# Optimization experiments

Measured on AMD Instinct MI355X. Metric: run time of the kernel, lower is better.

## Reference

```python
import jax, jax.numpy as jnp
import numpy as np
import jax.scipy.linalg

BATCH = 1048576
M_NUM = 2
DT = 0.0166667
NN_RATIO = 0.5
SLOPE = 0.01  # torch LeakyReLU default negative_slope


def setup_inputs() -> dict:
    key = jax.random.key(0)
    ks = jax.random.split(key, 16)
    inp = {}
    inp["SS"] = jax.random.normal(ks[0], (BATCH, 2), dtype=jnp.float32)
    inp["Alphas"] = jax.random.uniform(ks[1], (BATCH, M_NUM), dtype=jnp.float32)
    # per-muscle scalar parameters (positive so sqrt(K*I) is valid)
    inp["K0s"] = jax.random.uniform(ks[2], (M_NUM,), minval=0.5, maxval=1.5)
    inp["K1s"] = jax.random.uniform(ks[3], (M_NUM,), minval=0.5, maxval=1.5)
    inp["L0s"] = jax.random.uniform(ks[4], (M_NUM,), minval=0.5, maxval=1.5)
    inp["L1s"] = jax.random.uniform(ks[5], (M_NUM,), minval=0.1, maxval=0.6)
    inp["Ms"] = jnp.array([1.0, -1.0], dtype=jnp.float32)  # moment arms
    inp["I_p"] = jnp.array([1.0], dtype=jnp.float32)
    inp["B_p"] = jnp.array([0.05], dtype=jnp.float32)
    inp["K_p"] = jnp.array([1.0], dtype=jnp.float32)
    # per-muscle compensational MLP weights: 3-32-32-32-1 (eval mode, dropout off)
    s = 0.1
    inp["W1"] = jax.random.normal(ks[6], (M_NUM, 3, 32)) * s
    inp["b1"] = jax.random.normal(ks[7], (M_NUM, 32)) * s
    inp["W2"] = jax.random.normal(ks[8], (M_NUM, 32, 32)) * s
    inp["b2"] = jax.random.normal(ks[9], (M_NUM, 32)) * s
    inp["W3"] = jax.random.normal(ks[10], (M_NUM, 32, 32)) * s
    inp["b3"] = jax.random.normal(ks[11], (M_NUM, 32)) * s
    inp["W4"] = jax.random.normal(ks[12], (M_NUM, 32, 1)) * s
    inp["b4"] = jax.random.normal(ks[13], (M_NUM, 1)) * s
    return inp


def _leaky(x):
    return jnp.where(x >= 0, x, SLOPE * x)


def reference(SS, Alphas, K0s, K1s, L0s, L1s, Ms, I_p, B_p, K_p,
              W1, b1, W2, b2, W3, b3, W4, b4):
    B = SS.shape[0]
    a = jnp.clip(Alphas, 0.0, 1.0)                      # (B, m)
    # muscle length / speed via scalar moment arms
    l = SS[:, 0:1] * Ms[None, :]                        # (B, m)
    dl = SS[:, 1:2] * Ms[None, :]                       # (B, m)
    # compensational MLPs, vectorized over muscles
    x = jnp.stack([l, dl, a], axis=-1)                  # (B, m, 3)
    h = _leaky(jnp.einsum('bmi,mio->bmo', x, W1) + b1[None])
    h = _leaky(jnp.einsum('bmi,mio->bmo', h, W2) + b2[None])
    h = _leaky(jnp.einsum('bmi,mio->bmo', h, W3) + b3[None])
    nn_out = jnp.tanh(jnp.einsum('bmi,mio->bmo', h, W4) + b4[None])[..., 0] * NN_RATIO  # (B, m)

    I0, B0p, K0p = I_p[0], B_p[0], K_p[0]
    K_m = K0s[None, :] + K1s[None, :] * a               # (B, m)
    K_tot = jnp.sum(K_m * Ms[None, :] ** 2, axis=1)     # (B,)
    A10 = -(K_tot + K0p) / I0
    D = 2.0 * jnp.sqrt(K_tot * I0)
    A11 = -(D + B0p) / I0
    B_F = K_m * (L0s[None, :] + L1s[None, :] * a - jnp.abs(l)) \
        + K1s[None, :] * L1s[None, :] * a * a * nn_out   # (B, m)
    B10 = jnp.sum(B_F * Ms[None, :], axis=1) / I0       # (B,)

    # Build block matrix M6 = [[A*dt, B*dt, 0], [0, 0, I2], [0, 0, 0]]
    M6 = jnp.zeros((B, 6, 6), dtype=SS.dtype)
    M6 = M6.at[:, 0, 1].set(DT)
    M6 = M6.at[:, 1, 0].set(A10 * DT)
    M6 = M6.at[:, 1, 1].set(A11 * DT)
    M6 = M6.at[:, 1, 2].set(B10 * DT)
    M6 = M6.at[:, 1, 3].set(DT / I0)
    M6 = M6.at[:, 2, 4].set(1.0)
    M6 = M6.at[:, 3, 5].set(1.0)

    expMT = jax.vmap(jax.scipy.linalg.expm)(M6)         # (B, 6, 6)
    Ad = expMT[:, :2, :2]
    Bd1 = expMT[:, :2, 4:6]
    Bd0 = expMT[:, :2, 2:4] - Bd1
    u = jnp.array([1.0, 0.0], dtype=SS.dtype)           # U0 = U1 = [1, 0]
    SSout = (jnp.einsum('bij,bj->bi', Ad, SS)
             + jnp.einsum('bij,j->bi', Bd0, u)
             + jnp.einsum('bij,j->bi', Bd1, u))          # (B, 2)
    return SSout[:, :1], SSout
```

## Files before the change

kernel.cpp:

```cpp
#include <hip/hip_runtime.h>
#include <hip/hip_bf16.h>

#define NTHREADS 256
#define WAVES    4
#define GPW      4
#define DT_F     0.0166667f

typedef _Float16 f16x8 __attribute__((ext_vector_type(8)));
typedef _Float16 f16x4 __attribute__((ext_vector_type(4)));
typedef _Float16 f16x2 __attribute__((ext_vector_type(2)));
typedef float    f32x4 __attribute__((ext_vector_type(4)));

#define BF16_PROBE 0xBF803F80u

#define OW1 0
#define OB1 192
#define OW2 256
#define OB2 2368
#define OW3 2432
#define OB3 4544
#define OW4 4608
#define OB4 4672
#define SMEM_F 4680

__device__ __forceinline__ float leaky(float x) { return fmaxf(x, 0.01f * x); }

__device__ __forceinline__ float tanh_fast(float x) {
    const float xc = fminf(fmaxf(x, -10.0f), 10.0f);
    const float t  = __expf(2.0f * xc);
    return (t - 1.0f) * __builtin_amdgcn_rcpf(t + 1.0f);
}

__device__ __forceinline__ f16x2 pkrtz(float a, float b) {
    return __builtin_bit_cast(f16x2, __builtin_amdgcn_cvt_pkrtz(a, b));
}

__device__ __forceinline__ f16x4 leaky_cvt(const f32x4 D) {
    f16x2 lo = pkrtz(D[0], D[1]);
    f16x2 hi = pkrtz(D[2], D[3]);
    const f16x2 sl = {(_Float16)0.01f, (_Float16)0.01f};
    lo = __builtin_elementwise_max(lo, lo * sl);
    hi = __builtin_elementwise_max(hi, hi * sl);
    return __builtin_shufflevector(lo, hi, 0, 1, 2, 3);
}

__device__ __forceinline__ f16x4 bias_leaky_cvt(const f32x4 D, const f16x4 b) {
    f16x2 lo = pkrtz(D[0], D[1]);
    f16x2 hi = pkrtz(D[2], D[3]);
    const f16x2 blo = {b[0], b[1]};
    const f16x2 bhi = {b[2], b[3]};
    lo = lo + blo;
    hi = hi + bhi;
    const f16x2 sl = {(_Float16)0.01f, (_Float16)0.01f};
    lo = __builtin_elementwise_max(lo, lo * sl);
    hi = __builtin_elementwise_max(hi, hi * sl);
    return __builtin_shufflevector(lo, hi, 0, 1, 2, 3);
}

__device__ __forceinline__ f16x8 concat8(const f16x4 a, const f16x4 b) {
    return __builtin_shufflevector(a, b, 0, 1, 2, 3, 4, 5, 6, 7);
}

__device__ __forceinline__ void epilogue_math(
    const float* P, float ss0, float ss1, float a0, float a1,
    float nn0, float nn1, float& o0f, float& o1f)
{
    const float K00 = P[0], K01 = P[1], K10 = P[2], K11 = P[3];
    const float L00 = P[4], L01 = P[5], L10 = P[6], L11 = P[7];
    const float Ms0 = P[8], Ms1 = P[9];
    const float I0  = P[10], B0p = P[11], K0p = P[12];

    const float Km0   = fmaf(K10, a0, K00);
    const float Km1   = fmaf(K11, a1, K01);
    const float K_tot = Km0*Ms0*Ms0 + Km1*Ms1*Ms1;
    const float invI  = 1.0f / I0;
    const float A10   = -(K_tot + K0p) * invI;
    const float Dd    = 2.0f * sqrtf(K_tot * I0);
    const float A11   = -(Dd + B0p) * invI;
    const float absl0 = fabsf(ss0 * Ms0);
    const float absl1 = fabsf(ss0 * Ms1);
    const float BF0   = Km0 * (L00 + L10*a0 - absl0) + K10*L10*a0*a0*nn0;
    const float BF1   = Km1 * (L01 + L11*a1 - absl1) + K11*L11*a1*a1*nn1;
    const float B10   = (BF0*Ms0 + BF1*Ms1) * invI;

    const float t01 = DT_F;
    const float t10 = A10 * DT_F;
    const float t11 = A11 * DT_F;

    float p00 = 1.0f/120.0f, p01 = 0.0f, p10 = 0.0f, p11 = 1.0f/120.0f;
    const float coef[4] = {1.0f/24.0f, 1.0f/6.0f, 0.5f, 1.0f};
    #pragma unroll
    for (int j = 0; j < 4; ++j) {
        const float cj  = coef[j];
        const float n00 = p01*t10 + cj;
        const float n01 = p00*t01 + p01*t11;
        const float n10 = p11*t10;
        const float n11 = p10*t01 + p11*t11 + cj;
        p00 = n00; p01 = n01; p10 = n10; p11 = n11;
    }
    const float e00 = 1.0f + t01*p10;
    const float e01 = t01*p11;
    const float e10 = t10*p00 + t11*p10;
    const float e11 = 1.0f + t10*p01 + t11*p11;

    const float cscale = DT_F * B10;
    o0f = fmaf(e00, ss0, fmaf(e01, ss1, p01 * cscale));
    o1f = fmaf(e10, ss0, fmaf(e11, ss1, p11 * cscale));
}

__device__ __forceinline__ float ldb(const __hip_bfloat16* p, int i) {
    return __bfloat162float(p[i]);
}

__device__ void run_bf16_fallback(
    const void* SSv, const void* ALv, const void* K0sv, const void* K1sv,
    const void* L0sv, const void* L1sv, const void* Msv, const void* I_pv,
    const void* B_pv, const void* K_pv, const void* W1v, const void* b1v,
    const void* W2v, const void* b2v, const void* W3v, const void* b3v,
    const void* W4v, const void* b4v, void* outv, int batch)
{
    const __hip_bfloat16* SS = (const __hip_bfloat16*)SSv;
    const __hip_bfloat16* AL = (const __hip_bfloat16*)ALv;
    const __hip_bfloat16* W1 = (const __hip_bfloat16*)W1v;
    const __hip_bfloat16* b1 = (const __hip_bfloat16*)b1v;
    const __hip_bfloat16* W2 = (const __hip_bfloat16*)W2v;
    const __hip_bfloat16* b2 = (const __hip_bfloat16*)b2v;
    const __hip_bfloat16* W3 = (const __hip_bfloat16*)W3v;
    const __hip_bfloat16* b3 = (const __hip_bfloat16*)b3v;
    const __hip_bfloat16* W4 = (const __hip_bfloat16*)W4v;
    const __hip_bfloat16* b4 = (const __hip_bfloat16*)b4v;

    float P[13];
    P[0] = ldb((const __hip_bfloat16*)K0sv, 0); P[1] = ldb((const __hip_bfloat16*)K0sv, 1);
    P[2] = ldb((const __hip_bfloat16*)K1sv, 0); P[3] = ldb((const __hip_bfloat16*)K1sv, 1);
    P[4] = ldb((const __hip_bfloat16*)L0sv, 0); P[5] = ldb((const __hip_bfloat16*)L0sv, 1);
    P[6] = ldb((const __hip_bfloat16*)L1sv, 0); P[7] = ldb((const __hip_bfloat16*)L1sv, 1);
    P[8] = ldb((const __hip_bfloat16*)Msv, 0);  P[9] = ldb((const __hip_bfloat16*)Msv, 1);
    P[10] = ldb((const __hip_bfloat16*)I_pv, 0);
    P[11] = ldb((const __hip_bfloat16*)B_pv, 0);
    P[12] = ldb((const __hip_bfloat16*)K_pv, 0);

    const int stride = gridDim.x * blockDim.x;
    for (int e = blockIdx.x * blockDim.x + threadIdx.x; e < batch; e += stride) {
        const float ss0 = ldb(SS, 2*e), ss1 = ldb(SS, 2*e+1);
        float a0 = fminf(fmaxf(ldb(AL, 2*e),   0.0f), 1.0f);
        float a1 = fminf(fmaxf(ldb(AL, 2*e+1), 0.0f), 1.0f);
        float nn[2];
        #pragma unroll 1
        for (int m = 0; m < 2; ++m) {
            const float am = m ? a1 : a0;
            const float l = ss0 * P[8+m], dl = ss1 * P[8+m];
            float h[32];
            #pragma unroll
            for (int o = 0; o < 32; ++o)
                h[o] = leaky(fmaf(l, ldb(W1, m*96+o),
                             fmaf(dl, ldb(W1, m*96+32+o),
                             fmaf(am, ldb(W1, m*96+64+o), ldb(b1, m*32+o)))));
            float g[32];
            #pragma unroll 1
            for (int oc = 0; oc < 4; ++oc) {
                float acc[8];
                #pragma unroll
                for (int j = 0; j < 8; ++j) acc[j] = ldb(b2, m*32+oc*8+j);
                #pragma unroll
                for (int k = 0; k < 32; ++k) {
                    #pragma unroll
                    for (int j = 0; j < 8; ++j)
                        acc[j] = fmaf(h[k], ldb(W2, m*1024+k*32+oc*8+j), acc[j]);
                }
                #pragma unroll
                for (int j = 0; j < 8; ++j) g[oc*8+j] = leaky(acc[j]);
            }
            float h3[32];
            #pragma unroll 1
            for (int oc = 0; oc < 4; ++oc) {
                float acc[8];
                #pragma unroll
                for (int j = 0; j < 8; ++j) acc[j] = ldb(b3, m*32+oc*8+j);
                #pragma unroll
                for (int k = 0; k < 32; ++k) {
                    #pragma unroll
                    for (int j = 0; j < 8; ++j)
                        acc[j] = fmaf(g[k], ldb(W3, m*1024+k*32+oc*8+j), acc[j]);
                }
                #pragma unroll
                for (int j = 0; j < 8; ++j) h3[oc*8+j] = leaky(acc[j]);
            }
            float acc = ldb(b4, m);
            #pragma unroll
            for (int k = 0; k < 32; ++k) acc = fmaf(h3[k], ldb(W4, m*32+k), acc);
            nn[m] = tanh_fast(acc) * 0.5f;
        }
        float o0f, o1f;
        epilogue_math(P, ss0, ss1, a0, a1, nn[0], nn[1], o0f, o1f);
        __hip_bfloat16* out0 = (__hip_bfloat16*)outv;
        __hip_bfloat162* out1 = (__hip_bfloat162*)(out0 + batch);
        out0[e] = __float2bfloat16(o0f);
        __hip_bfloat162 pr;
        pr.x = __float2bfloat16(o0f);
        pr.y = __float2bfloat16(o1f);
        out1[e] = pr;
    }
}

__global__ __launch_bounds__(NTHREADS, 3) void joint_kernel(
    const void* __restrict__ SSv, const void* __restrict__ ALv,
    const void* __restrict__ K0sv, const void* __restrict__ K1sv,
    const void* __restrict__ L0sv, const void* __restrict__ L1sv,
    const void* __restrict__ Msv,  const void* __restrict__ I_pv,
    const void* __restrict__ B_pv, const void* __restrict__ K_pv,
    const void* __restrict__ W1v,  const void* __restrict__ b1v,
    const void* __restrict__ W2v,  const void* __restrict__ b2v,
    const void* __restrict__ W3v,  const void* __restrict__ b3v,
    const void* __restrict__ W4v,  const void* __restrict__ b4v,
    void* __restrict__ outv, int batch)
{
    const unsigned probe = *(const unsigned*)Msv;
    if (probe == BF16_PROBE) {
        run_bf16_fallback(SSv, ALv, K0sv, K1sv, L0sv, L1sv, Msv, I_pv, B_pv,
                          K_pv, W1v, b1v, W2v, b2v, W3v, b3v, W4v, b4v,
                          outv, batch);
        return;
    }

    const float* SS = (const float*)SSv;
    const float* AL = (const float*)ALv;
    const float* W1 = (const float*)W1v;  const float* b1 = (const float*)b1v;
    const float* W2 = (const float*)W2v;  const float* b2 = (const float*)b2v;
    const float* W3 = (const float*)W3v;  const float* b3 = (const float*)b3v;
    const float* W4 = (const float*)W4v;  const float* b4 = (const float*)b4v;

    const int tid  = threadIdx.x;
    const int wave = tid >> 6;
    const int lane = tid & 63;
    const int n    = lane & 15;
    const int q    = lane >> 4;
    const int gh0  = ((n >> 2) << 3) + (n & 3);

    __shared__ __align__(16) float sm[SMEM_F];
    for (int i = tid; i < 192;  i += NTHREADS) sm[OW1+i] = W1[i];
    for (int i = tid; i < 2048; i += NTHREADS) {
        const int mi = i >> 10, rem = i & 1023, in = rem >> 5, out = rem & 31;
        sm[OW2 + mi*1056 + in*33 + out] = W2[i];
        sm[OW3 + mi*1056 + in*33 + out] = W3[i];
    }
    for (int i = tid; i < 64;   i += NTHREADS) {
        sm[OB1+i] = b1[i]; sm[OB2+i] = b2[i];
        sm[OB3+i] = b3[i]; sm[OW4+i] = W4[i];
    }
    if (tid < 2) sm[OB4+tid] = b4[tid];
    __syncthreads();

    f16x4 A1[2][2];
    #pragma unroll
    for (int mi = 0; mi < 2; ++mi)
        #pragma unroll
        for (int h = 0; h < 2; ++h)
            #pragma unroll
            for (int j = 0; j < 4; ++j) {
                const int k = q*4 + j;
                const int g = gh0 + h*4;
                float v = 0.0f;
                if (k < 3)       v = sm[OW1 + mi*96 + k*32 + g];
                else if (k == 3) v = sm[OB1 + mi*32 + g];
                A1[mi][h][j] = (_Float16)v;
            }
    f16x8 A2[2][2], A3[2][2];
    #pragma unroll
    for (int mi = 0; mi < 2; ++mi)
        #pragma unroll
        for (int h = 0; h < 2; ++h) {
            const int g = gh0 + h*4;
            #pragma unroll
            for (int j = 0; j < 8; ++j) {
                const int in = q*8 + j;
                A2[mi][h][j] = (_Float16)sm[OW2 + mi*1056 + in*33 + g];
                A3[mi][h][j] = (_Float16)sm[OW3 + mi*1056 + in*33 + g];
            }
        }
    f16x8 A4[2];
    #pragma unroll
    for (int mi = 0; mi < 2; ++mi)
        #pragma unroll
        for (int j = 0; j < 8; ++j)
            A4[mi][j] = (_Float16)sm[OW4 + mi*32 + q*8 + j];
    f16x4 Bs2[2][2], Bs3[2][2];
    #pragma unroll
    for (int mi = 0; mi < 2; ++mi)
        #pragma unroll
        for (int h = 0; h < 2; ++h)
            #pragma unroll
            for (int r = 0; r < 4; ++r) {
                Bs2[mi][h][r] = (_Float16)sm[OB2 + mi*32 + q*8 + h*4 + r];
                Bs3[mi][h][r] = (_Float16)sm[OB3 + mi*32 + q*8 + h*4 + r];
            }
    const float b4s0 = sm[OB4], b4s1 = sm[OB4+1];

    float P[13];
    P[0]  = ((const float*)K0sv)[0]; P[1]  = ((const float*)K0sv)[1];
    P[2]  = ((const float*)K1sv)[0]; P[3]  = ((const float*)K1sv)[1];
    P[4]  = ((const float*)L0sv)[0]; P[5]  = ((const float*)L0sv)[1];
    P[6]  = ((const float*)L1sv)[0]; P[7]  = ((const float*)L1sv)[1];
    P[8]  = ((const float*)Msv)[0];  P[9]  = ((const float*)Msv)[1];
    P[10] = ((const float*)I_pv)[0];
    P[11] = ((const float*)B_pv)[0];
    P[12] = ((const float*)K_pv)[0];

    const f32x4 zero = {0.0f, 0.0f, 0.0f, 0.0f};
    const int groupBase = (blockIdx.x * WAVES + wave) * GPW;

    #pragma unroll 1
    for (int g = 0; g < GPW; ++g) {
        const int ebase = (groupBase + g) * 64;
        float my_r0 = 0.0f, my_r1 = 0.0f;

        #pragma unroll 1
        for (int p = 0; p < 2; ++p) {
            float2 s[2];
            float a0c[2], a1c[2];
            #pragma unroll
            for (int ti = 0; ti < 2; ++ti) {
                const int e  = ebase + (2*p + ti)*16 + n;
                const int eg = min(e, batch - 1);
                s[ti] = ((const float2*)SS)[eg];
                const float2 al = ((const float2*)AL)[eg];
                a0c[ti] = fminf(fmaxf(al.x, 0.0f), 1.0f);
                a1c[ti] = fminf(fmaxf(al.y, 0.0f), 1.0f);
            }

            f16x4 B1[2][2];
            #pragma unroll
            for (int ti = 0; ti < 2; ++ti)
                #pragma unroll
                for (int mi = 0; mi < 2; ++mi) {
                    const float Msm = P[8 + mi];
                    const float am  = mi ? a1c[ti] : a0c[ti];
                    const f16x2 blo = pkrtz(s[ti].x * Msm, s[ti].y * Msm);
                    const f16x2 bhi = pkrtz(am, 1.0f);
                    B1[ti][mi] = __builtin_shufflevector(blo, bhi, 0, 1, 2, 3);
                }

            f16x8 Bx[2][2];
            #pragma unroll
            for (int ti = 0; ti < 2; ++ti)
                #pragma unroll
                for (int mi = 0; mi < 2; ++mi) {
                    const f32x4 d0 = __builtin_amdgcn_mfma_f32_16x16x16f16(A1[mi][0], B1[ti][mi], zero, 0, 0, 0);
                    const f32x4 d1 = __builtin_amdgcn_mfma_f32_16x16x16f16(A1[mi][1], B1[ti][mi], zero, 0, 0, 0);
                    Bx[ti][mi] = concat8(leaky_cvt(d0), leaky_cvt(d1));
                }

            #pragma unroll
            for (int ti = 0; ti < 2; ++ti)
                #pragma unroll
                for (int mi = 0; mi < 2; ++mi) {
                    const f32x4 d0 = __builtin_amdgcn_mfma_f32_16x16x32_f16(A2[mi][0], Bx[ti][mi], zero, 0, 0, 0);
                    const f32x4 d1 = __builtin_amdgcn_mfma_f32_16x16x32_f16(A2[mi][1], Bx[ti][mi], zero, 0, 0, 0);
                    Bx[ti][mi] = concat8(bias_leaky_cvt(d0, Bs2[mi][0]),
                                         bias_leaky_cvt(d1, Bs2[mi][1]));
                }

            #pragma unroll
            for (int ti = 0; ti < 2; ++ti)
                #pragma unroll
                for (int mi = 0; mi < 2; ++mi) {
                    const f32x4 d0 = __builtin_amdgcn_mfma_f32_16x16x32_f16(A3[mi][0], Bx[ti][mi], zero, 0, 0, 0);
                    const f32x4 d1 = __builtin_amdgcn_mfma_f32_16x16x32_f16(A3[mi][1], Bx[ti][mi], zero, 0, 0, 0);
                    Bx[ti][mi] = concat8(bias_leaky_cvt(d0, Bs3[mi][0]),
                                         bias_leaky_cvt(d1, Bs3[mi][1]));
                }

            #pragma unroll
            for (int ti = 0; ti < 2; ++ti) {
                const bool own = (q == (2*p + ti));
                #pragma unroll
                for (int mi = 0; mi < 2; ++mi) {
                    f32x4 G = __builtin_amdgcn_mfma_f32_16x16x32_f16(A4[mi], Bx[ti][mi], zero, 0, 0, 0);
                    const float r = G[0] + (mi ? b4s1 : b4s0);
                    if (mi == 0) my_r0 = own ? r : my_r0;
                    else         my_r1 = own ? r : my_r1;
                }
            }
        }

        const int eo  = ebase + lane;
        const int eog = min(eo, batch - 1);
        const float2 se  = ((const float2*)SS)[eog];
        const float2 ale = ((const float2*)AL)[eog];
        const float a0 = fminf(fmaxf(ale.x, 0.0f), 1.0f);
        const float a1 = fminf(fmaxf(ale.y, 0.0f), 1.0f);
        const float nn0 = tanh_fast(my_r0) * 0.5f;
        const float nn1 = tanh_fast(my_r1) * 0.5f;
        float o0f, o1f;
        epilogue_math(P, se.x, se.y, a0, a1, nn0, nn1, o0f, o1f);
        if (eo < batch) {
            ((float*)outv)[eo] = o0f;
            ((float2*)((float*)outv + batch))[eo] = make_float2(o0f, o1f);
        }
    }
}

extern "C" void kernel_launch(void* const* d_in, const int* in_sizes, int n_in,
                              void* d_out, int out_size, void* d_ws, size_t ws_size,
                              hipStream_t stream) {
    const int batch = in_sizes[0] / 2;
    const int elemsPerBlock = 64 * GPW * WAVES;
    const int grid = (batch + elemsPerBlock - 1) / elemsPerBlock;
    joint_kernel<<<grid, NTHREADS, 0, stream>>>(
        d_in[0], d_in[1], d_in[2], d_in[3], d_in[4], d_in[5], d_in[6],
        d_in[7], d_in[8], d_in[9], d_in[10], d_in[11], d_in[12], d_in[13],
        d_in[14], d_in[15], d_in[16], d_in[17], d_out, batch);
}
```

Before: 117.5 us.

## Stream pre-swizzled f16 MLP weights from LDS per layer to raise occupancy

Each block now converts the MLP weights and biases to f16 in LDS once, already in the per-lane MFMA fragment layout. Each layer then reads them with volatile vector LDS loads just before use, instead of keeping every weight fragment in registers for the whole kernel. This lowers register pressure, so the launch bound goes from 3 to 8 blocks per CU, and GPW drops from 4 to 2 so more blocks are launched. The cost is extra LDS traffic on every group iteration and more blocks paying the weight-staging prologue.

```diff
diff --git a/kernel.cpp b/kernel.cpp
--- a/kernel.cpp
+++ b/kernel.cpp
@@ -3,7 +3,7 @@
 
 #define NTHREADS 256
 #define WAVES    4
-#define GPW      4
+#define GPW      2
 #define DT_F     0.0166667f
 
 typedef _Float16 f16x8 __attribute__((ext_vector_type(8)));
@@ -13,15 +13,13 @@
 
 #define BF16_PROBE 0xBF803F80u
 
-#define OW1 0
-#define OB1 192
-#define OW2 256
-#define OB2 2368
-#define OW3 2432
-#define OB3 4544
-#define OW4 4608
-#define OB4 4672
-#define SMEM_F 4680
+#define A1T 0
+#define B2T 1024
+#define B3T 2048
+#define A4T 3072
+#define A2T 4096
+#define A3T 6144
+#define SMH_F16 8192
 
 __device__ __forceinline__ float leaky(float x) { return fmaxf(x, 0.01f * x); }
 
@@ -59,6 +57,13 @@
 
 __device__ __forceinline__ f16x8 concat8(const f16x4 a, const f16x4 b) {
     return __builtin_shufflevector(a, b, 0, 1, 2, 3, 4, 5, 6, 7);
+}
+
+__device__ __forceinline__ f16x4 ldsv4(const _Float16* p) {
+    return *(const volatile f16x4*)p;
+}
+__device__ __forceinline__ f16x8 ldsv8(const _Float16* p) {
+    return *(const volatile f16x8*)p;
 }
 
 __device__ __forceinline__ void epilogue_math(
@@ -203,7 +208,7 @@
     }
 }
 
-__global__ __launch_bounds__(NTHREADS, 3) void joint_kernel(
+__global__ __launch_bounds__(NTHREADS, 8) void joint_kernel(
     const void* __restrict__ SSv, const void* __restrict__ ALv,
     const void* __restrict__ K0sv, const void* __restrict__ K1sv,
     const void* __restrict__ L0sv, const void* __restrict__ L1sv,
@@ -235,66 +240,41 @@
     const int lane = tid & 63;
     const int n    = lane & 15;
     const int q    = lane >> 4;
-    const int gh0  = ((n >> 2) << 3) + (n & 3);
-
-    __shared__ __align__(16) float sm[SMEM_F];
-    for (int i = tid; i < 192;  i += NTHREADS) sm[OW1+i] = W1[i];
+
+    __shared__ __align__(16) _Float16 smh[SMH_F16];
+    __shared__ float sb4[2];
+
     for (int i = tid; i < 2048; i += NTHREADS) {
         const int mi = i >> 10, rem = i & 1023, in = rem >> 5, out = rem & 31;
-        sm[OW2 + mi*1056 + in*33 + out] = W2[i];
-        sm[OW3 + mi*1056 + in*33 + out] = W3[i];
-    }
-    for (int i = tid; i < 64;   i += NTHREADS) {
-        sm[OB1+i] = b1[i]; sm[OB2+i] = b2[i];
-        sm[OB3+i] = b3[i]; sm[OW4+i] = W4[i];
-    }
-    if (tid < 2) sm[OB4+tid] = b4[tid];
+        const int qq = in >> 3, j = in & 7, h = (out >> 2) & 1;
+        const int nn_ = ((out >> 3) << 2) | (out & 3);
+        const int l  = (qq << 4) | nn_;
+        smh[A2T + ((mi*2 + h)*64 + l)*8 + j] = (_Float16)W2[i];
+        smh[A3T + ((mi*2 + h)*64 + l)*8 + j] = (_Float16)W3[i];
+    }
+    for (int i = tid; i < 1024; i += NTHREADS) {
+        const int mi = i >> 9, h = (i >> 8) & 1, l = (i >> 2) & 63, j = i & 3;
+        const int qq = l >> 4, nn_ = l & 15;
+        const int gg = ((nn_ >> 2) << 3) + (nn_ & 3) + h*4;
+        const int k  = qq*4 + j;
+        float v = 0.0f;
+        if (k < 3)       v = W1[mi*96 + k*32 + gg];
+        else if (k == 3) v = b1[mi*32 + gg];
+        smh[A1T + ((mi*2 + h)*64 + l)*4 + j] = (_Float16)v;
+    }
+    for (int i = tid; i < 1024; i += NTHREADS) {
+        const int mi = i >> 9, l = (i >> 3) & 63, j = i & 7;
+        smh[A4T + (mi*64 + l)*8 + j] = (_Float16)W4[mi*32 + (l >> 4)*8 + j];
+    }
+    for (int i = tid; i < 1024; i += NTHREADS) {
+        const int mi = i >> 9, h = (i >> 8) & 1, l = (i >> 2) & 63, r = i & 3;
+        smh[B2T + ((mi*2 + h)*64 + l)*4 + r] = (_Float16)b2[mi*32 + (l >> 4)*8 + h*4 + r];
+        smh[B3T + ((mi*2 + h)*64 + l)*4 + r] = (_Float16)b3[mi*32 + (l >> 4)*8 + h*4 + r];
+    }
+    if (tid < 2) sb4[tid] = b4[tid];
     __syncthreads();
 
-    f16x4 A1[2][2];
-    #pragma unroll
-    for (int mi = 0; mi < 2; ++mi)
-        #pragma unroll
-        for (int h = 0; h < 2; ++h)
-            #pragma unroll
-            for (int j = 0; j < 4; ++j) {
-                const int k = q*4 + j;
-                const int g = gh0 + h*4;
-                float v = 0.0f;
-                if (k < 3)       v = sm[OW1 + mi*96 + k*32 + g];
-                else if (k == 3) v = sm[OB1 + mi*32 + g];
-                A1[mi][h][j] = (_Float16)v;
-            }
-    f16x8 A2[2][2], A3[2][2];
-    #pragma unroll
-    for (int mi = 0; mi < 2; ++mi)
-        #pragma unroll
-        for (int h = 0; h < 2; ++h) {
-            const int g = gh0 + h*4;
-            #pragma unroll
-            for (int j = 0; j < 8; ++j) {
-                const int in = q*8 + j;
-                A2[mi][h][j] = (_Float16)sm[OW2 + mi*1056 + in*33 + g];
-                A3[mi][h][j] = (_Float16)sm[OW3 + mi*1056 + in*33 + g];
-            }
-        }
-    f16x8 A4[2];
-    #pragma unroll
-    for (int mi = 0; mi < 2; ++mi)
-        #pragma unroll
-        for (int j = 0; j < 8; ++j)
-            A4[mi][j] = (_Float16)sm[OW4 + mi*32 + q*8 + j];
-    f16x4 Bs2[2][2], Bs3[2][2];
-    #pragma unroll
-    for (int mi = 0; mi < 2; ++mi)
-        #pragma unroll
-        for (int h = 0; h < 2; ++h)
-            #pragma unroll
-            for (int r = 0; r < 4; ++r) {
-                Bs2[mi][h][r] = (_Float16)sm[OB2 + mi*32 + q*8 + h*4 + r];
-                Bs3[mi][h][r] = (_Float16)sm[OB3 + mi*32 + q*8 + h*4 + r];
-            }
-    const float b4s0 = sm[OB4], b4s1 = sm[OB4+1];
+    const float b4s0 = sb4[0], b4s1 = sb4[1];
 
     float P[13];
     P[0]  = ((const float*)K0sv)[0]; P[1]  = ((const float*)K0sv)[1];
@@ -341,44 +321,77 @@
                 }
 
             f16x8 Bx[2][2];
-            #pragma unroll
-            for (int ti = 0; ti < 2; ++ti)
-                #pragma unroll
-                for (int mi = 0; mi < 2; ++mi) {
-                    const f32x4 d0 = __builtin_amdgcn_mfma_f32_16x16x16f16(A1[mi][0], B1[ti][mi], zero, 0, 0, 0);
-                    const f32x4 d1 = __builtin_amdgcn_mfma_f32_16x16x16f16(A1[mi][1], B1[ti][mi], zero, 0, 0, 0);
-                    Bx[ti][mi] = concat8(leaky_cvt(d0), leaky_cvt(d1));
-                }
-
-            #pragma unroll
-            for (int ti = 0; ti < 2; ++ti)
-                #pragma unroll
-                for (int mi = 0; mi < 2; ++mi) {
-                    const f32x4 d0 = __builtin_amdgcn_mfma_f32_16x16x32_f16(A2[mi][0], Bx[ti][mi], zero, 0, 0, 0);
-                    const f32x4 d1 = __builtin_amdgcn_mfma_f32_16x16x32_f16(A2[mi][1], Bx[ti][mi], zero, 0, 0, 0);
-                    Bx[ti][mi] = concat8(bias_leaky_cvt(d0, Bs2[mi][0]),
-                                         bias_leaky_cvt(d1, Bs2[mi][1]));
-                }
-
-            #pragma unroll
-            for (int ti = 0; ti < 2; ++ti)
-                #pragma unroll
-                for (int mi = 0; mi < 2; ++mi) {
-                    const f32x4 d0 = __builtin_amdgcn_mfma_f32_16x16x32_f16(A3[mi][0], Bx[ti][mi], zero, 0, 0, 0);
-                    const f32x4 d1 = __builtin_amdgcn_mfma_f32_16x16x32_f16(A3[mi][1], Bx[ti][mi], zero, 0, 0, 0);
-                    Bx[ti][mi] = concat8(bias_leaky_cvt(d0, Bs3[mi][0]),
-                                         bias_leaky_cvt(d1, Bs3[mi][1]));
-                }
-
-            #pragma unroll
-            for (int ti = 0; ti < 2; ++ti) {
-                const bool own = (q == (2*p + ti));
-                #pragma unroll
-                for (int mi = 0; mi < 2; ++mi) {
-                    f32x4 G = __builtin_amdgcn_mfma_f32_16x16x32_f16(A4[mi], Bx[ti][mi], zero, 0, 0, 0);
-                    const float r = G[0] + (mi ? b4s1 : b4s0);
-                    if (mi == 0) my_r0 = own ? r : my_r0;
-                    else         my_r1 = own ? r : my_r1;
+            {
+                f16x4 A1f[2][2];
+                #pragma unroll
+                for (int mi = 0; mi < 2; ++mi)
+                    #pragma unroll
+                    for (int h = 0; h < 2; ++h)
+                        A1f[mi][h] = ldsv4(&smh[A1T + ((mi*2 + h)*64 + lane)*4]);
+                #pragma unroll
+                for (int ti = 0; ti < 2; ++ti)
+                    #pragma unroll
+                    for (int mi = 0; mi < 2; ++mi) {
+                        const f32x4 d0 = __builtin_amdgcn_mfma_f32_16x16x16f16(A1f[mi][0], B1[ti][mi], zero, 0, 0, 0);
+                        const f32x4 d1 = __builtin_amdgcn_mfma_f32_16x16x16f16(A1f[mi][1], B1[ti][mi], zero, 0, 0, 0);
+                        Bx[ti][mi] = concat8(leaky_cvt(d0), leaky_cvt(d1));
+                    }
+            }
+            {
+                f16x8 A2f[2][2];
+                f16x4 B2f[2][2];
+                #pragma unroll
+                for (int mi = 0; mi < 2; ++mi)
+                    #pragma unroll
+                    for (int h = 0; h < 2; ++h) {
+                        A2f[mi][h] = ldsv8(&smh[A2T + ((mi*2 + h)*64 + lane)*8]);
+                        B2f[mi][h] = ldsv4(&smh[B2T + ((mi*2 + h)*64 + lane)*4]);
+                    }
+                #pragma unroll
+                for (int ti = 0; ti < 2; ++ti)
+                    #pragma unroll
+                    for (int mi = 0; mi < 2; ++mi) {
+                        const f32x4 d0 = __builtin_amdgcn_mfma_f32_16x16x32_f16(A2f[mi][0], Bx[ti][mi], zero, 0, 0, 0);
+                        const f32x4 d1 = __builtin_amdgcn_mfma_f32_16x16x32_f16(A2f[mi][1], Bx[ti][mi], zero, 0, 0, 0);
+                        Bx[ti][mi] = concat8(bias_leaky_cvt(d0, B2f[mi][0]),
+                                             bias_leaky_cvt(d1, B2f[mi][1]));
+                    }
+            }
+            {
+                f16x8 A3f[2][2];
+                f16x4 B3f[2][2];
+                #pragma unroll
+                for (int mi = 0; mi < 2; ++mi)
+                    #pragma unroll
+                    for (int h = 0; h < 2; ++h) {
+                        A3f[mi][h] = ldsv8(&smh[A3T + ((mi*2 + h)*64 + lane)*8]);
+                        B3f[mi][h] = ldsv4(&smh[B3T + ((mi*2 + h)*64 + lane)*4]);
+                    }
+                #pragma unroll
+                for (int ti = 0; ti < 2; ++ti)
+                    #pragma unroll
+                    for (int mi = 0; mi < 2; ++mi) {
+                        const f32x4 d0 = __builtin_amdgcn_mfma_f32_16x16x32_f16(A3f[mi][0], Bx[ti][mi], zero, 0, 0, 0);
+                        const f32x4 d1 = __builtin_amdgcn_mfma_f32_16x16x32_f16(A3f[mi][1], Bx[ti][mi], zero, 0, 0, 0);
+                        Bx[ti][mi] = concat8(bias_leaky_cvt(d0, B3f[mi][0]),
+                                             bias_leaky_cvt(d1, B3f[mi][1]));
+                    }
+            }
+            {
+                f16x8 A4f[2];
+                #pragma unroll
+                for (int mi = 0; mi < 2; ++mi)
+                    A4f[mi] = ldsv8(&smh[A4T + (mi*64 + lane)*8]);
+                #pragma unroll
+                for (int ti = 0; ti < 2; ++ti) {
+                    const bool own = (q == (2*p + ti));
+                    #pragma unroll
+                    for (int mi = 0; mi < 2; ++mi) {
+                        f32x4 G = __builtin_amdgcn_mfma_f32_16x16x32_f16(A4f[mi], Bx[ti][mi], zero, 0, 0, 0);
+                        const float r = G[0] + (mi ? b4s1 : b4s0);
+                        if (mi == 0) my_r0 = own ? r : my_r0;
+                        else         my_r1 = own ? r : my_r1;
+                    }
                 }
             }
         }
```

Measured after the change: 209.8 us. 78.6% more time.
